# Optimization experiments

Hardware: AMD Instinct MI355X
Metric: run time of the kernel (lower is better)

Reference implementation:

```python
import jax, jax.numpy as jnp
import numpy as np

N_NODES = 100000
N_EDGES = 3200000
IN_C, HID_C, OUT_C = 128, 64, 64


def setup_inputs() -> dict:
    key = jax.random.key(0)
    k = jax.random.split(key, 6)
    x = jax.random.normal(k[0], (N_NODES, IN_C), dtype=jnp.float32)
    edge_index = jax.random.randint(k[1], (2, N_EDGES), 0, N_NODES, dtype=jnp.int64)
    edge_weight = jax.random.uniform(k[2], (N_EDGES,), dtype=jnp.float32)
    W1 = jax.random.normal(k[3], (IN_C, HID_C), dtype=jnp.float32) * (1.0 / np.sqrt(IN_C))
    b1 = jnp.zeros((HID_C,), dtype=jnp.float32)
    W2 = jax.random.normal(k[4], (HID_C, OUT_C), dtype=jnp.float32) * (1.0 / np.sqrt(HID_C))
    b2 = jnp.zeros((OUT_C,), dtype=jnp.float32)
    return {"x": x, "edge_index": edge_index, "edge_weight": edge_weight,
            "W1": W1, "b1": b1, "W2": W2, "b2": b2}


def _gcn_norm(edge_index, edge_weight, num_nodes, dtype):
    # PyG GCNConv default: add self-loops (weight 1), symmetric normalization
    loop = jnp.arange(num_nodes, dtype=edge_index.dtype)
    row = jnp.concatenate([edge_index[0], loop])  # sources
    col = jnp.concatenate([edge_index[1], loop])  # targets (aggregation dim)
    w = jnp.concatenate([edge_weight.astype(dtype), jnp.ones((num_nodes,), dtype)])
    deg = jax.ops.segment_sum(w, col, num_segments=num_nodes)
    deg_inv_sqrt = jnp.where(deg > 0, jax.lax.rsqrt(deg), jnp.zeros((), dtype))
    norm = deg_inv_sqrt[row] * w * deg_inv_sqrt[col]
    return row, col, norm


def _gcn_conv(h, row, col, norm, W, b, num_nodes):
    h = h @ W                      # [N, C_out]
    msg = h[row] * norm[:, None]   # gather over sources, scale by edge norm
    out = jax.ops.segment_sum(msg, col, num_segments=num_nodes)  # scatter-add to targets
    return out + b


def reference(x, edge_index, edge_weight, W1, b1, W2, b2):
    num_nodes = x.shape[0]
    row, col, norm = _gcn_norm(edge_index, edge_weight, num_nodes, x.dtype)
    h = _gcn_conv(x, row, col, norm, W1, b1, num_nodes)
    h = jax.nn.relu(h)
    return _gcn_conv(h, row, col, norm, W2, b2, num_nodes)
```

## Files before the change

kernel.cpp:

```cpp
#include <hip/hip_runtime.h>
#include <hip/hip_bf16.h>

#define N_NODES 100000
#define N_EDGES 3200000
#define IN_C 128
#define HID_C 64
#define OUT_C 64

#define NBUCKET 196
#define SC_EDGES 4096
#define SC_GRID 782
#define CAP 18432

struct EdgeRec { int s; float v; };

typedef float f32x2 __attribute__((ext_vector_type(2)));
typedef float f32x4 __attribute__((ext_vector_type(4)));
typedef short bf16x8 __attribute__((ext_vector_type(8)));
union F8 { uint4 u; bf16x8 f; };

__device__ __forceinline__ unsigned pack_bf16(float lo, float hi) {
    unsigned short l = __hip_bfloat16_raw(__float2bfloat16(lo)).x;
    unsigned short h = __hip_bfloat16_raw(__float2bfloat16(hi)).x;
    return ((unsigned)h << 16) | l;
}
__device__ __forceinline__ float bf_lo(unsigned u) {
    union { unsigned u; float f; } c; c.u = u << 16; return c.f;
}
__device__ __forceinline__ float bf_hi(unsigned u) {
    union { unsigned u; float f; } c; c.u = u & 0xffff0000u; return c.f;
}
__device__ __forceinline__ f32x2 bfp(unsigned u) {
    union { unsigned u; float f; } lo, hi;
    lo.u = u << 16; hi.u = u & 0xffff0000u;
    f32x2 r; r.x = lo.f; r.y = hi.f; return r;
}
__device__ __forceinline__ void pk_fma(f32x2& acc, f32x2 a, f32x2 w) {
    asm("v_pk_fma_f32 %0, %1, %2, %0" : "+v"(acc) : "v"(a), "v"(w));
}
__device__ __forceinline__ void edge_acc(f32x2* acc2, uint4 u, float w) {
    f32x2 wv; wv.x = w; wv.y = w;
    pk_fma(acc2[0], bfp(u.x), wv);
    pk_fma(acc2[1], bfp(u.y), wv);
    pk_fma(acc2[2], bfp(u.z), wv);
    pk_fma(acc2[3], bfp(u.w), wv);
}
__device__ __forceinline__ unsigned cvt_pk_bf16(float lo, float hi) {
    unsigned r;
    asm("v_cvt_pk_bf16_f32 %0, %1, %2" : "=v"(r) : "v"(lo), "v"(hi));
    return r;
}
__device__ __forceinline__ void split_frag(const float* f, uint4& hi4, uint4& lo4) {
    unsigned hi[4], lo[4];
    #pragma unroll
    for (int p = 0; p < 4; ++p) {
        hi[p] = cvt_pk_bf16(f[2 * p], f[2 * p + 1]);
        float r0 = f[2 * p]     - bf_lo(hi[p]);
        float r1 = f[2 * p + 1] - bf_hi(hi[p]);
        lo[p] = cvt_pk_bf16(r0, r1);
    }
    hi4 = make_uint4(hi[0], hi[1], hi[2], hi[3]);
    lo4 = make_uint4(lo[0], lo[1], lo[2], lo[3]);
}

__global__ __launch_bounds__(256) void scatter_coarse(const int* __restrict__ ei,
                                                      const float* __restrict__ ew,
                                                      int* __restrict__ gcursor,
                                                      uint2* __restrict__ tmp) {
    __shared__ int hist[256];
    __shared__ int scan[256];
    __shared__ int lcur[256];
    __shared__ int adj[256];
    __shared__ uint2 rec[SC_EDGES];
    __shared__ unsigned char bk[SC_EDGES];
    int tid = threadIdx.x;
    hist[tid] = 0;
    __syncthreads();
    int base = blockIdx.x * SC_EDGES;
    unsigned ys[16];
    float    ws[16];
    int      bs[16];
    for (int i = 0; i < 16; ++i) {
        int e = base + i * 256 + tid;
        if (e < N_EDGES) {
            int t = ei[N_EDGES + e];
            bs[i] = t >> 9;
            ys[i] = (unsigned)ei[e] | ((unsigned)(t & 511) << 17);
            ws[i] = ew[e];
            atomicAdd(&hist[bs[i]], 1);
        } else bs[i] = -1;
    }
    __syncthreads();
    int v = hist[tid];
    scan[tid] = v;
    __syncthreads();
    for (int off = 1; off < 256; off <<= 1) {
        int t = scan[tid];
        int add = (tid >= off) ? scan[tid - off] : 0;
        __syncthreads();
        scan[tid] = t + add;
        __syncthreads();
    }
    int excl = scan[tid] - v;
    int gb = (v > 0) ? atomicAdd(&gcursor[tid], v) : 0;
    lcur[tid] = excl;
    adj[tid] = tid * CAP + gb - excl;
    __syncthreads();
    for (int i = 0; i < 16; ++i) {
        if (bs[i] >= 0) {
            int j = atomicAdd(&lcur[bs[i]], 1);
            rec[j] = make_uint2(__float_as_uint(ws[i]), ys[i]);
            bk[j] = (unsigned char)bs[i];
        }
    }
    __syncthreads();
    int count = N_EDGES - base;
    if (count > SC_EDGES) count = SC_EDGES;
    for (int j = tid; j < count; j += 256) {
        int b = bk[j];
        tmp[adj[b] + j] = rec[j];
    }
}

__global__ __launch_bounds__(256) void bucket_scan(const int* __restrict__ gcnt,
                                                   int* __restrict__ start) {
    __shared__ int s[256];
    int tid = threadIdx.x;
    int v = gcnt[tid];
    s[tid] = v;
    __syncthreads();
    for (int off = 1; off < 256; off <<= 1) {
        int t = s[tid];
        int add = (tid >= off) ? s[tid - off] : 0;
        __syncthreads();
        s[tid] = t + add;
        __syncthreads();
    }
    start[tid] = s[tid] - v;
    if (tid == 255) start[256] = s[255];
}

__global__ __launch_bounds__(512) void fine_sort(const int* __restrict__ start,
                                                 const uint2* __restrict__ tmpPad,
                                                 int* __restrict__ rowptr,
                                                 float* __restrict__ dis,
                                                 EdgeRec* __restrict__ ed) {
    __shared__ int   cnt[512];
    __shared__ float wdeg[512];
    __shared__ int   s[512];
    int tid = threadIdx.x;
    int nodeBase = blockIdx.x << 9;
    int bb = start[blockIdx.x];
    int nEdge = start[blockIdx.x + 1] - bb;
    const uint2* tb = tmpPad + (size_t)blockIdx.x * CAP;
    cnt[tid] = 0;
    wdeg[tid] = 0.f;
    __syncthreads();
    for (int e = tid; e < nEdge; e += 512) {
        uint2 r = tb[e];
        int l = (r.y >> 17) & 511;
        atomicAdd(&cnt[l], 1);
        atomicAdd(&wdeg[l], __uint_as_float(r.x));
    }
    __syncthreads();
    int v = cnt[tid];
    s[tid] = v;
    __syncthreads();
    for (int off = 1; off < 512; off <<= 1) {
        int t = s[tid];
        int add = (tid >= off) ? s[tid - off] : 0;
        __syncthreads();
        s[tid] = t + add;
        __syncthreads();
    }
    int excl = s[tid] - v;
    int node = nodeBase + tid;
    if (node < N_NODES) {
        rowptr[node] = bb + excl;
        dis[node] = rsqrtf(wdeg[tid] + 1.0f);
    }
    if (node == N_NODES) rowptr[N_NODES] = N_EDGES;
    cnt[tid] = excl;
    __syncthreads();
    for (int e = tid; e < nEdge; e += 512) {
        uint2 r = tb[e];
        int l = (r.y >> 17) & 511;
        int p = atomicAdd(&cnt[l], 1);
        EdgeRec o;
        o.s = (int)(r.y & 0x1FFFFu);
        o.v = __uint_as_float(r.x);
        ed[bb + p] = o;
    }
}

template<int K>
__global__ __launch_bounds__(256) void mm_mfma(const float* __restrict__ X,
                                               const float* __restrict__ W,
                                               const float* __restrict__ dis,
                                               unsigned* __restrict__ h) {
    constexpr int NKS = K / 32;
    int wv = threadIdx.x >> 6;
    int l  = threadIdx.x & 63;
    int lr = l & 15;
    int kr = l >> 4;
    int col = wv * 16 + lr;
    int row0 = blockIdx.x * 16;
    const float* xbase = X + (size_t)(row0 + lr) * K + kr * 8;
    float4 xa[NKS], xb[NKS];
    #pragma unroll
    for (int ks = 0; ks < NKS; ++ks) {
        const float4* xp = (const float4*)(xbase + ks * 32);
        xa[ks] = xp[0];
        xb[ks] = xp[1];
    }
    F8 bhi[NKS], blo[NKS];
    #pragma unroll
    for (int ks = 0; ks < NKS; ++ks) {
        const float* wp = W + (ks * 32 + kr * 8) * 64 + col;
        float f[8];
        #pragma unroll
        for (int j = 0; j < 8; ++j) f[j] = wp[j * 64];
        split_frag(f, bhi[ks].u, blo[ks].u);
    }
    f32x4 acc = {0.f, 0.f, 0.f, 0.f};
    #pragma unroll
    for (int ks = 0; ks < NKS; ++ks) {
        float f[8] = {xa[ks].x, xa[ks].y, xa[ks].z, xa[ks].w,
                      xb[ks].x, xb[ks].y, xb[ks].z, xb[ks].w};
        F8 ahi, alo;
        split_frag(f, ahi.u, alo.u);
        acc = __builtin_amdgcn_mfma_f32_16x16x32_bf16(ahi.f, bhi[ks].f, acc, 0, 0, 0);
        acc = __builtin_amdgcn_mfma_f32_16x16x32_bf16(ahi.f, blo[ks].f, acc, 0, 0, 0);
        acc = __builtin_amdgcn_mfma_f32_16x16x32_bf16(alo.f, bhi[ks].f, acc, 0, 0, 0);
    }
    int rbase = row0 + kr * 4;
    float v0 = acc[0] * dis[rbase + 0];
    float v1 = acc[1] * dis[rbase + 1];
    float v2 = acc[2] * dis[rbase + 2];
    float v3 = acc[3] * dis[rbase + 3];
    float o0 = __shfl_xor(v0, 1, 64);
    float o1 = __shfl_xor(v1, 1, 64);
    float o2 = __shfl_xor(v2, 1, 64);
    float o3 = __shfl_xor(v3, 1, 64);
    if ((lr & 1) == 0) {
        int ci = col >> 1;
        h[(rbase + 0) * 32 + ci] = pack_bf16(v0, o0);
        h[(rbase + 1) * 32 + ci] = pack_bf16(v1, o1);
        h[(rbase + 2) * 32 + ci] = pack_bf16(v2, o2);
        h[(rbase + 3) * 32 + ci] = pack_bf16(v3, o3);
    }
}

__global__ __launch_bounds__(256, 8) void agg_kernel(const int* __restrict__ rowptr,
                                                     const EdgeRec* __restrict__ ed,
                                                     const unsigned* __restrict__ h,
                                                     const float* __restrict__ dis,
                                                     const float* __restrict__ b,
                                                     float* __restrict__ out,
                                                     int relu) {
    int node = blockIdx.x * 4 + (threadIdx.x >> 6);
    int lane = threadIdx.x & 63;
    int g = lane >> 3;
    int cl = lane & 7;
    int beg = rowptr[node];
    int end = rowptr[node + 1];
    const uint4* h16 = (const uint4*)h;
    const char*  hb  = (const char*)h + (size_t)cl * 16;
    float d  = dis[node];
    uint4 us = h16[(size_t)node * 8 + cl];
    f32x2 acc2[4];
    acc2[0] = 0.f; acc2[1] = 0.f; acc2[2] = 0.f; acc2[3] = 0.f;
    int n = end - beg;
    int nb = (n + 31) >> 5;
    int nm1 = n - 1;
    uint2 q0, q1, q2, q3;
    if (nb > 0) {
        q0 = *(const uint2*)(ed + beg + min(g,      nm1));
        q1 = *(const uint2*)(ed + beg + min(g + 8,  nm1));
        q2 = *(const uint2*)(ed + beg + min(g + 16, nm1));
        q3 = *(const uint2*)(ed + beg + min(g + 24, nm1));
        for (int bt = 0; bt < nb; ++bt) {
            int ob = (bt << 5) + g;
            float w0 = (ob      < n) ? __uint_as_float(q0.y) : 0.f;
            float w1 = (ob + 8  < n) ? __uint_as_float(q1.y) : 0.f;
            float w2 = (ob + 16 < n) ? __uint_as_float(q2.y) : 0.f;
            float w3 = (ob + 24 < n) ? __uint_as_float(q3.y) : 0.f;
            uint4 u0 = *(const uint4*)(hb + ((size_t)(unsigned)q0.x << 7));
            uint4 u1 = *(const uint4*)(hb + ((size_t)(unsigned)q1.x << 7));
            uint4 u2 = *(const uint4*)(hb + ((size_t)(unsigned)q2.x << 7));
            uint4 u3 = *(const uint4*)(hb + ((size_t)(unsigned)q3.x << 7));
            if (bt + 1 < nb) {
                int on = ob + 32;
                q0 = *(const uint2*)(ed + beg + min(on,      nm1));
                q1 = *(const uint2*)(ed + beg + min(on + 8,  nm1));
                q2 = *(const uint2*)(ed + beg + min(on + 16, nm1));
                q3 = *(const uint2*)(ed + beg + min(on + 24, nm1));
            }
            edge_acc(acc2, u0, w0);
            edge_acc(acc2, u1, w1);
            edge_acc(acc2, u2, w2);
            edge_acc(acc2, u3, w3);
        }
    }
    float acc[8] = { acc2[0].x, acc2[0].y, acc2[1].x, acc2[1].y,
                     acc2[2].x, acc2[2].y, acc2[3].x, acc2[3].y };
    #pragma unroll
    for (int kk = 0; kk < 8; ++kk) {
        acc[kk] += __shfl_xor(acc[kk], 8, 64);
        acc[kk] += __shfl_xor(acc[kk], 16, 64);
        acc[kk] += __shfl_xor(acc[kk], 32, 64);
    }
    if (g == 0) {
        float hs[8] = { bf_lo(us.x), bf_hi(us.x), bf_lo(us.y), bf_hi(us.y),
                        bf_lo(us.z), bf_hi(us.z), bf_lo(us.w), bf_hi(us.w) };
        const float4* b4 = (const float4*)b;
        float4 bv0 = b4[cl * 2], bv1 = b4[cl * 2 + 1];
        float4 v0, v1;
        v0.x = d * (acc[0] + hs[0]) + bv0.x;
        v0.y = d * (acc[1] + hs[1]) + bv0.y;
        v0.z = d * (acc[2] + hs[2]) + bv0.z;
        v0.w = d * (acc[3] + hs[3]) + bv0.w;
        v1.x = d * (acc[4] + hs[4]) + bv1.x;
        v1.y = d * (acc[5] + hs[5]) + bv1.y;
        v1.z = d * (acc[6] + hs[6]) + bv1.z;
        v1.w = d * (acc[7] + hs[7]) + bv1.w;
        if (relu) {
            v0.x = fmaxf(v0.x, 0.f); v0.y = fmaxf(v0.y, 0.f);
            v0.z = fmaxf(v0.z, 0.f); v0.w = fmaxf(v0.w, 0.f);
            v1.x = fmaxf(v1.x, 0.f); v1.y = fmaxf(v1.y, 0.f);
            v1.z = fmaxf(v1.z, 0.f); v1.w = fmaxf(v1.w, 0.f);
        }
        float4* o4 = (float4*)out;
        o4[node * 16 + cl * 2]     = v0;
        o4[node * 16 + cl * 2 + 1] = v1;
    }
}

extern "C" void kernel_launch(void* const* d_in, const int* in_sizes, int n_in,
                              void* d_out, int out_size, void* d_ws, size_t ws_size,
                              hipStream_t stream) {
    const float* x  = (const float*)d_in[0];
    const int*   ei = (const int*)d_in[1];
    const float* ew = (const float*)d_in[2];
    const float* W1 = (const float*)d_in[3];
    const float* b1 = (const float*)d_in[4];
    const float* W2 = (const float*)d_in[5];
    const float* b2 = (const float*)d_in[6];
    float* out = (float*)d_out;

    char* p = (char*)d_ws;
    auto carve = [&](size_t bytes) { char* r = p; p += (bytes + 255) & ~(size_t)255; return r; };
    float*    dis     = (float*)carve(N_NODES * 4);
    int*      rowptr  = (int*)carve((N_NODES + 1) * 4);
    int*      start   = (int*)carve(257 * 4);
    int*      gcursor = (int*)carve(256 * 4);
    EdgeRec*  ed      = (EdgeRec*)carve((size_t)N_EDGES * 8);
    size_t    r2sz    = (size_t)NBUCKET * CAP * 8;
    size_t    hasz    = (size_t)N_NODES * 64 * 6;
    char*     r2      = carve(r2sz > hasz ? r2sz : hasz);
    uint2*    tmpPad  = (uint2*)r2;
    unsigned* h       = (unsigned*)r2;
    float*    a       = (float*)(r2 + (size_t)N_NODES * 64 * 2);

    hipMemsetAsync(gcursor, 0, 256 * sizeof(int), stream);
    scatter_coarse<<<SC_GRID, 256, 0, stream>>>(ei, ew, gcursor, tmpPad);
    bucket_scan<<<1, 256, 0, stream>>>(gcursor, start);
    fine_sort<<<NBUCKET, 512, 0, stream>>>(start, tmpPad, rowptr, dis, ed);

    mm_mfma<IN_C><<<N_NODES / 16, 256, 0, stream>>>(x, W1, dis, h);
    agg_kernel<<<N_NODES / 4, 256, 0, stream>>>(rowptr, ed, h, dis, b1, a, 1);

    mm_mfma<HID_C><<<N_NODES / 16, 256, 0, stream>>>(a, W2, dis, h);
    agg_kernel<<<N_NODES / 4, 256, 0, stream>>>(rowptr, ed, h, dis, b2, out, 0);
}
```

Baseline: 359.3 us.

## Compute degrees with global atomics and fuse first GEMM into coarse scatter

Adds a pass that computes per-node edge counts and weighted degrees with global atomics up front. The first matmul no longer waits on the sort, so its tiles run as extra blocks in the same launch as the coarse bucket scatter, overlapping compute with the scatter's memory traffic. The fine sort drops its counting pass and reads the precomputed counts, and later kernels recompute rsqrt from the weighted degree instead of reading a stored dis array. The trade is millions of contended global atomics and an extra read of the edge arrays, plus a larger workspace so h no longer aliases the scatter buffer.

Result: slower. 609.9 us (+69.8%).

```diff
diff --git a/kernel.cpp b/kernel.cpp
--- a/kernel.cpp
+++ b/kernel.cpp
@@ -11,6 +11,7 @@
 #define SC_EDGES 4096
 #define SC_GRID 782
 #define CAP 18432
+#define MM1_GRID (N_NODES / 16)
 
 struct EdgeRec { int s; float v; };
 
@@ -63,16 +64,96 @@
     lo4 = make_uint4(lo[0], lo[1], lo[2], lo[3]);
 }
 
-__global__ __launch_bounds__(256) void scatter_coarse(const int* __restrict__ ei,
-                                                      const float* __restrict__ ew,
-                                                      int* __restrict__ gcursor,
-                                                      uint2* __restrict__ tmp) {
+__global__ __launch_bounds__(256) void deg_kernel(const int* __restrict__ ei,
+                                                  const float* __restrict__ ew,
+                                                  int* __restrict__ deg,
+                                                  float* __restrict__ wdeg) {
+    int gid = blockIdx.x * 256 + threadIdx.x;
+    int4   t = ((const int4*)(ei + N_EDGES))[gid];
+    float4 w = ((const float4*)ew)[gid];
+    atomicAdd(&deg[t.x], 1); atomicAdd(&wdeg[t.x], w.x);
+    atomicAdd(&deg[t.y], 1); atomicAdd(&wdeg[t.y], w.y);
+    atomicAdd(&deg[t.z], 1); atomicAdd(&wdeg[t.z], w.z);
+    atomicAdd(&deg[t.w], 1); atomicAdd(&wdeg[t.w], w.w);
+}
+
+template<int K>
+__device__ __forceinline__ void mm_tile(int tile,
+                                        const float* __restrict__ X,
+                                        const float* __restrict__ W,
+                                        const float* __restrict__ wdeg,
+                                        unsigned* __restrict__ h) {
+    constexpr int NKS = K / 32;
+    int wv = threadIdx.x >> 6;
+    int l  = threadIdx.x & 63;
+    int lr = l & 15;
+    int kr = l >> 4;
+    int col = wv * 16 + lr;
+    int row0 = tile * 16;
+    const float* xbase = X + (size_t)(row0 + lr) * K + kr * 8;
+    float4 xa[NKS], xb[NKS];
+    #pragma unroll
+    for (int ks = 0; ks < NKS; ++ks) {
+        const float4* xp = (const float4*)(xbase + ks * 32);
+        xa[ks] = xp[0];
+        xb[ks] = xp[1];
+    }
+    F8 bhi[NKS], blo[NKS];
+    #pragma unroll
+    for (int ks = 0; ks < NKS; ++ks) {
+        const float* wp = W + (ks * 32 + kr * 8) * 64 + col;
+        float f[8];
+        #pragma unroll
+        for (int j = 0; j < 8; ++j) f[j] = wp[j * 64];
+        split_frag(f, bhi[ks].u, blo[ks].u);
+    }
+    f32x4 acc = {0.f, 0.f, 0.f, 0.f};
+    #pragma unroll
+    for (int ks = 0; ks < NKS; ++ks) {
+        float f[8] = {xa[ks].x, xa[ks].y, xa[ks].z, xa[ks].w,
+                      xb[ks].x, xb[ks].y, xb[ks].z, xb[ks].w};
+        F8 ahi, alo;
+        split_frag(f, ahi.u, alo.u);
+        acc = __builtin_amdgcn_mfma_f32_16x16x32_bf16(ahi.f, bhi[ks].f, acc, 0, 0, 0);
+        acc = __builtin_amdgcn_mfma_f32_16x16x32_bf16(ahi.f, blo[ks].f, acc, 0, 0, 0);
+        acc = __builtin_amdgcn_mfma_f32_16x16x32_bf16(alo.f, bhi[ks].f, acc, 0, 0, 0);
+    }
+    int rbase = row0 + kr * 4;
+    float v0 = acc[0] * rsqrtf(wdeg[rbase + 0] + 1.0f);
+    float v1 = acc[1] * rsqrtf(wdeg[rbase + 1] + 1.0f);
+    float v2 = acc[2] * rsqrtf(wdeg[rbase + 2] + 1.0f);
+    float v3 = acc[3] * rsqrtf(wdeg[rbase + 3] + 1.0f);
+    float o0 = __shfl_xor(v0, 1, 64);
+    float o1 = __shfl_xor(v1, 1, 64);
+    float o2 = __shfl_xor(v2, 1, 64);
+    float o3 = __shfl_xor(v3, 1, 64);
+    if ((lr & 1) == 0) {
+        int ci = col >> 1;
+        h[(rbase + 0) * 32 + ci] = pack_bf16(v0, o0);
+        h[(rbase + 1) * 32 + ci] = pack_bf16(v1, o1);
+        h[(rbase + 2) * 32 + ci] = pack_bf16(v2, o2);
+        h[(rbase + 3) * 32 + ci] = pack_bf16(v3, o3);
+    }
+}
+
+__global__ __launch_bounds__(256) void fused_scatter_mm1(const int* __restrict__ ei,
+                                                         const float* __restrict__ ew,
+                                                         int* __restrict__ gcursor,
+                                                         uint2* __restrict__ tmp,
+                                                         const float* __restrict__ x,
+                                                         const float* __restrict__ W1,
+                                                         const float* __restrict__ wdeg,
+                                                         unsigned* __restrict__ h) {
     __shared__ int hist[256];
     __shared__ int scan[256];
     __shared__ int lcur[256];
     __shared__ int adj[256];
     __shared__ uint2 rec[SC_EDGES];
     __shared__ unsigned char bk[SC_EDGES];
+    if (blockIdx.x >= SC_GRID) {
+        mm_tile<IN_C>(blockIdx.x - SC_GRID, x, W1, wdeg, h);
+        return;
+    }
     int tid = threadIdx.x;
     hist[tid] = 0;
     __syncthreads();
@@ -122,6 +203,14 @@
     }
 }
 
+template<int K>
+__global__ __launch_bounds__(256) void mm_mfma(const float* __restrict__ X,
+                                               const float* __restrict__ W,
+                                               const float* __restrict__ wdeg,
+                                               unsigned* __restrict__ h) {
+    mm_tile<K>(blockIdx.x, X, W, wdeg, h);
+}
+
 __global__ __launch_bounds__(256) void bucket_scan(const int* __restrict__ gcnt,
                                                    int* __restrict__ start) {
     __shared__ int s[256];
@@ -140,30 +229,20 @@
     if (tid == 255) start[256] = s[255];
 }
 
-__global__ __launch_bounds__(512) void fine_sort(const int* __restrict__ start,
-                                                 const uint2* __restrict__ tmpPad,
-                                                 int* __restrict__ rowptr,
-                                                 float* __restrict__ dis,
-                                                 EdgeRec* __restrict__ ed) {
-    __shared__ int   cnt[512];
-    __shared__ float wdeg[512];
-    __shared__ int   s[512];
+__global__ __launch_bounds__(512) void fine_place(const int* __restrict__ start,
+                                                  const int* __restrict__ deg,
+                                                  const uint2* __restrict__ tmpPad,
+                                                  int* __restrict__ rowptr,
+                                                  EdgeRec* __restrict__ ed) {
+    __shared__ int cnt[512];
+    __shared__ int s[512];
     int tid = threadIdx.x;
     int nodeBase = blockIdx.x << 9;
     int bb = start[blockIdx.x];
     int nEdge = start[blockIdx.x + 1] - bb;
     const uint2* tb = tmpPad + (size_t)blockIdx.x * CAP;
-    cnt[tid] = 0;
-    wdeg[tid] = 0.f;
-    __syncthreads();
-    for (int e = tid; e < nEdge; e += 512) {
-        uint2 r = tb[e];
-        int l = (r.y >> 17) & 511;
-        atomicAdd(&cnt[l], 1);
-        atomicAdd(&wdeg[l], __uint_as_float(r.x));
-    }
-    __syncthreads();
-    int v = cnt[tid];
+    int node = nodeBase + tid;
+    int v = (node < N_NODES) ? deg[node] : 0;
     s[tid] = v;
     __syncthreads();
     for (int off = 1; off < 512; off <<= 1) {
@@ -174,11 +253,7 @@
         __syncthreads();
     }
     int excl = s[tid] - v;
-    int node = nodeBase + tid;
-    if (node < N_NODES) {
-        rowptr[node] = bb + excl;
-        dis[node] = rsqrtf(wdeg[tid] + 1.0f);
-    }
+    if (node < N_NODES) rowptr[node] = bb + excl;
     if (node == N_NODES) rowptr[N_NODES] = N_EDGES;
     cnt[tid] = excl;
     __syncthreads();
@@ -193,68 +268,10 @@
     }
 }
 
-template<int K>
-__global__ __launch_bounds__(256) void mm_mfma(const float* __restrict__ X,
-                                               const float* __restrict__ W,
-                                               const float* __restrict__ dis,
-                                               unsigned* __restrict__ h) {
-    constexpr int NKS = K / 32;
-    int wv = threadIdx.x >> 6;
-    int l  = threadIdx.x & 63;
-    int lr = l & 15;
-    int kr = l >> 4;
-    int col = wv * 16 + lr;
-    int row0 = blockIdx.x * 16;
-    const float* xbase = X + (size_t)(row0 + lr) * K + kr * 8;
-    float4 xa[NKS], xb[NKS];
-    #pragma unroll
-    for (int ks = 0; ks < NKS; ++ks) {
-        const float4* xp = (const float4*)(xbase + ks * 32);
-        xa[ks] = xp[0];
-        xb[ks] = xp[1];
-    }
-    F8 bhi[NKS], blo[NKS];
-    #pragma unroll
-    for (int ks = 0; ks < NKS; ++ks) {
-        const float* wp = W + (ks * 32 + kr * 8) * 64 + col;
-        float f[8];
-        #pragma unroll
-        for (int j = 0; j < 8; ++j) f[j] = wp[j * 64];
-        split_frag(f, bhi[ks].u, blo[ks].u);
-    }
-    f32x4 acc = {0.f, 0.f, 0.f, 0.f};
-    #pragma unroll
-    for (int ks = 0; ks < NKS; ++ks) {
-        float f[8] = {xa[ks].x, xa[ks].y, xa[ks].z, xa[ks].w,
-                      xb[ks].x, xb[ks].y, xb[ks].z, xb[ks].w};
-        F8 ahi, alo;
-        split_frag(f, ahi.u, alo.u);
-        acc = __builtin_amdgcn_mfma_f32_16x16x32_bf16(ahi.f, bhi[ks].f, acc, 0, 0, 0);
-        acc = __builtin_amdgcn_mfma_f32_16x16x32_bf16(ahi.f, blo[ks].f, acc, 0, 0, 0);
-        acc = __builtin_amdgcn_mfma_f32_16x16x32_bf16(alo.f, bhi[ks].f, acc, 0, 0, 0);
-    }
-    int rbase = row0 + kr * 4;
-    float v0 = acc[0] * dis[rbase + 0];
-    float v1 = acc[1] * dis[rbase + 1];
-    float v2 = acc[2] * dis[rbase + 2];
-    float v3 = acc[3] * dis[rbase + 3];
-    float o0 = __shfl_xor(v0, 1, 64);
-    float o1 = __shfl_xor(v1, 1, 64);
-    float o2 = __shfl_xor(v2, 1, 64);
-    float o3 = __shfl_xor(v3, 1, 64);
-    if ((lr & 1) == 0) {
-        int ci = col >> 1;
-        h[(rbase + 0) * 32 + ci] = pack_bf16(v0, o0);
-        h[(rbase + 1) * 32 + ci] = pack_bf16(v1, o1);
-        h[(rbase + 2) * 32 + ci] = pack_bf16(v2, o2);
-        h[(rbase + 3) * 32 + ci] = pack_bf16(v3, o3);
-    }
-}
-
 __global__ __launch_bounds__(256, 8) void agg_kernel(const int* __restrict__ rowptr,
                                                      const EdgeRec* __restrict__ ed,
                                                      const unsigned* __restrict__ h,
-                                                     const float* __restrict__ dis,
+                                                     const float* __restrict__ wdeg,
                                                      const float* __restrict__ b,
                                                      float* __restrict__ out,
                                                      int relu) {
@@ -266,7 +283,7 @@
     int end = rowptr[node + 1];
     const uint4* h16 = (const uint4*)h;
     const char*  hb  = (const char*)h + (size_t)cl * 16;
-    float d  = dis[node];
+    float d  = rsqrtf(wdeg[node] + 1.0f);
     uint4 us = h16[(size_t)node * 8 + cl];
     f32x2 acc2[4];
     acc2[0] = 0.f; acc2[1] = 0.f; acc2[2] = 0.f; acc2[3] = 0.f;
@@ -350,26 +367,32 @@
 
     char* p = (char*)d_ws;
     auto carve = [&](size_t bytes) { char* r = p; p += (bytes + 255) & ~(size_t)255; return r; };
-    float*    dis     = (float*)carve(N_NODES * 4);
     int*      rowptr  = (int*)carve((N_NODES + 1) * 4);
     int*      start   = (int*)carve(257 * 4);
+    char*     z0      = p;
     int*      gcursor = (int*)carve(256 * 4);
+    int*      deg     = (int*)carve(N_NODES * 4);
+    float*    wdeg    = (float*)carve(N_NODES * 4);
+    size_t    zbytes  = (size_t)(p - z0);
     EdgeRec*  ed      = (EdgeRec*)carve((size_t)N_EDGES * 8);
+    unsigned* h       = (unsigned*)carve((size_t)N_NODES * 64 * 2);
     size_t    r2sz    = (size_t)NBUCKET * CAP * 8;
-    size_t    hasz    = (size_t)N_NODES * 64 * 6;
-    char*     r2      = carve(r2sz > hasz ? r2sz : hasz);
+    size_t    asz     = (size_t)N_NODES * 64 * 4;
+    char*     r2      = carve(r2sz > asz ? r2sz : asz);
     uint2*    tmpPad  = (uint2*)r2;
-    unsigned* h       = (unsigned*)r2;
-    float*    a       = (float*)(r2 + (size_t)N_NODES * 64 * 2);
-
-    hipMemsetAsync(gcursor, 0, 256 * sizeof(int), stream);
-    scatter_coarse<<<SC_GRID, 256, 0, stream>>>(ei, ew, gcursor, tmpPad);
+    float*    a       = (float*)r2;
+
+    hipMemsetAsync(z0, 0, zbytes, stream);
+
+    deg_kernel<<<N_EDGES / 1024, 256, 0, stream>>>(ei, ew, deg, wdeg);
+
+    fused_scatter_mm1<<<SC_GRID + MM1_GRID, 256, 0, stream>>>(ei, ew, gcursor,
+                                                              tmpPad, x, W1, wdeg, h);
     bucket_scan<<<1, 256, 0, stream>>>(gcursor, start);
-    fine_sort<<<NBUCKET, 512, 0, stream>>>(start, tmpPad, rowptr, dis, ed);
-
-    mm_mfma<IN_C><<<N_NODES / 16, 256, 0, stream>>>(x, W1, dis, h);
-    agg_kernel<<<N_NODES / 4, 256, 0, stream>>>(rowptr, ed, h, dis, b1, a, 1);
-
-    mm_mfma<HID_C><<<N_NODES / 16, 256, 0, stream>>>(a, W2, dis, h);
-    agg_kernel<<<N_NODES / 4, 256, 0, stream>>>(rowptr, ed, h, dis, b2, out, 0);
-}
+    fine_place<<<NBUCKET, 512, 0, stream>>>(start, deg, tmpPad, rowptr, ed);
+
+    agg_kernel<<<N_NODES / 4, 256, 0, stream>>>(rowptr, ed, h, wdeg, b1, a, 1);
+
+    mm_mfma<HID_C><<<N_NODES / 16, 256, 0, stream>>>(a, W2, wdeg, h);
+    agg_kernel<<<N_NODES / 4, 256, 0, stream>>>(rowptr, ed, h, wdeg, b2, out, 0);
+}
```

## Fuse first GEMM with edge scatter and fold source degree into edge weights

Applied to the files above, without the earlier changes.

The first projection X@W1 no longer depends on the degree normalization, so it runs as extra blocks inside the coarse edge-scatter launch, letting compute and the memory-bound scatter overlap. The source-side dis factor moves out of the GEMM epilogue into a new placement kernel that premultiplies each edge weight by dis[src]. The self-loop term is scaled by d in the aggregation instead. The fine sort splits into a count kernel and a place kernel, which adds a launch and re-reads tmpPad. The second GEMM uses a grid-stride loop with 1250 blocks and loads the weight fragments once per block.

After: 357.2 us. No clear change (-0.6%).

```diff
diff --git a/kernel.cpp b/kernel.cpp
--- a/kernel.cpp
+++ b/kernel.cpp
@@ -9,8 +9,10 @@
 
 #define NBUCKET 196
 #define SC_EDGES 4096
-#define SC_GRID 782
+#define SC_PER   (SC_EDGES / 256)
+#define SC_GRID  782
 #define CAP 18432
+#define MM1_GRID (N_NODES / 16)
 
 struct EdgeRec { int s; float v; };
 
@@ -63,24 +65,21 @@
     lo4 = make_uint4(lo[0], lo[1], lo[2], lo[3]);
 }
 
-__global__ __launch_bounds__(256) void scatter_coarse(const int* __restrict__ ei,
-                                                      const float* __restrict__ ew,
-                                                      int* __restrict__ gcursor,
-                                                      uint2* __restrict__ tmp) {
-    __shared__ int hist[256];
-    __shared__ int scan[256];
-    __shared__ int lcur[256];
-    __shared__ int adj[256];
-    __shared__ uint2 rec[SC_EDGES];
-    __shared__ unsigned char bk[SC_EDGES];
+__device__ __forceinline__ void scatter_body(const int* __restrict__ ei,
+                                             const float* __restrict__ ew,
+                                             int* __restrict__ gcursor,
+                                             uint2* __restrict__ tmp,
+                                             int* hist, int* scn, int* lcur,
+                                             int* adj, uint2* rec,
+                                             unsigned char* bk) {
     int tid = threadIdx.x;
     hist[tid] = 0;
     __syncthreads();
     int base = blockIdx.x * SC_EDGES;
-    unsigned ys[16];
-    float    ws[16];
-    int      bs[16];
-    for (int i = 0; i < 16; ++i) {
+    unsigned ys[SC_PER];
+    float    ws[SC_PER];
+    int      bs[SC_PER];
+    for (int i = 0; i < SC_PER; ++i) {
         int e = base + i * 256 + tid;
         if (e < N_EDGES) {
             int t = ei[N_EDGES + e];
@@ -92,21 +91,21 @@
     }
     __syncthreads();
     int v = hist[tid];
-    scan[tid] = v;
+    scn[tid] = v;
     __syncthreads();
     for (int off = 1; off < 256; off <<= 1) {
-        int t = scan[tid];
-        int add = (tid >= off) ? scan[tid - off] : 0;
-        __syncthreads();
-        scan[tid] = t + add;
-        __syncthreads();
-    }
-    int excl = scan[tid] - v;
+        int t = scn[tid];
+        int add = (tid >= off) ? scn[tid - off] : 0;
+        __syncthreads();
+        scn[tid] = t + add;
+        __syncthreads();
+    }
+    int excl = scn[tid] - v;
     int gb = (v > 0) ? atomicAdd(&gcursor[tid], v) : 0;
     lcur[tid] = excl;
     adj[tid] = tid * CAP + gb - excl;
     __syncthreads();
-    for (int i = 0; i < 16; ++i) {
+    for (int i = 0; i < SC_PER; ++i) {
         if (bs[i] >= 0) {
             int j = atomicAdd(&lcur[bs[i]], 1);
             rec[j] = make_uint2(__float_as_uint(ws[i]), ys[i]);
@@ -120,6 +119,101 @@
         int b = bk[j];
         tmp[adj[b] + j] = rec[j];
     }
+}
+
+template<int K>
+__device__ __forceinline__ void mm_tile_bf(int tile,
+                                           const float* __restrict__ X,
+                                           const F8* bhi, const F8* blo,
+                                           int lr, int kr, int col,
+                                           unsigned* __restrict__ h) {
+    constexpr int NKS = K / 32;
+    int row0 = tile * 16;
+    const float* xbase = X + (size_t)(row0 + lr) * K + kr * 8;
+    float4 xa[NKS], xb[NKS];
+    #pragma unroll
+    for (int ks = 0; ks < NKS; ++ks) {
+        const float4* xp = (const float4*)(xbase + ks * 32);
+        xa[ks] = xp[0];
+        xb[ks] = xp[1];
+    }
+    f32x4 acc = {0.f, 0.f, 0.f, 0.f};
+    #pragma unroll
+    for (int ks = 0; ks < NKS; ++ks) {
+        float f[8] = {xa[ks].x, xa[ks].y, xa[ks].z, xa[ks].w,
+                      xb[ks].x, xb[ks].y, xb[ks].z, xb[ks].w};
+        F8 ahi, alo;
+        split_frag(f, ahi.u, alo.u);
+        acc = __builtin_amdgcn_mfma_f32_16x16x32_bf16(ahi.f, bhi[ks].f, acc, 0, 0, 0);
+        acc = __builtin_amdgcn_mfma_f32_16x16x32_bf16(ahi.f, blo[ks].f, acc, 0, 0, 0);
+        acc = __builtin_amdgcn_mfma_f32_16x16x32_bf16(alo.f, bhi[ks].f, acc, 0, 0, 0);
+    }
+    int rbase = row0 + kr * 4;
+    float v0 = acc[0], v1 = acc[1], v2 = acc[2], v3 = acc[3];
+    float o0 = __shfl_xor(v0, 1, 64);
+    float o1 = __shfl_xor(v1, 1, 64);
+    float o2 = __shfl_xor(v2, 1, 64);
+    float o3 = __shfl_xor(v3, 1, 64);
+    if ((lr & 1) == 0) {
+        int ci = col >> 1;
+        h[(rbase + 0) * 32 + ci] = pack_bf16(v0, o0);
+        h[(rbase + 1) * 32 + ci] = pack_bf16(v1, o1);
+        h[(rbase + 2) * 32 + ci] = pack_bf16(v2, o2);
+        h[(rbase + 3) * 32 + ci] = pack_bf16(v3, o3);
+    }
+}
+
+template<int K>
+__device__ __forceinline__ void load_bfrags(const float* __restrict__ W,
+                                            int kr, int col, F8* bhi, F8* blo) {
+    #pragma unroll
+    for (int ks = 0; ks < K / 32; ++ks) {
+        const float* wp = W + (ks * 32 + kr * 8) * 64 + col;
+        float f[8];
+        #pragma unroll
+        for (int j = 0; j < 8; ++j) f[j] = wp[j * 64];
+        split_frag(f, bhi[ks].u, blo[ks].u);
+    }
+}
+
+__global__ __launch_bounds__(256) void fused_scatter_mm1(const int* __restrict__ ei,
+                                                         const float* __restrict__ ew,
+                                                         int* __restrict__ gcursor,
+                                                         uint2* __restrict__ tmp,
+                                                         const float* __restrict__ x,
+                                                         const float* __restrict__ W1,
+                                                         unsigned* __restrict__ h) {
+    __shared__ int hist[256];
+    __shared__ int scn[256];
+    __shared__ int lcur[256];
+    __shared__ int adj[256];
+    __shared__ uint2 rec[SC_EDGES];
+    __shared__ unsigned char bk[SC_EDGES];
+    if (blockIdx.x >= SC_GRID) {
+        int l  = threadIdx.x & 63;
+        int lr = l & 15;
+        int kr = l >> 4;
+        int col = (threadIdx.x >> 6) * 16 + lr;
+        F8 bhi[IN_C / 32], blo[IN_C / 32];
+        load_bfrags<IN_C>(W1, kr, col, bhi, blo);
+        mm_tile_bf<IN_C>(blockIdx.x - SC_GRID, x, bhi, blo, lr, kr, col, h);
+        return;
+    }
+    scatter_body(ei, ew, gcursor, tmp, hist, scn, lcur, adj, rec, bk);
+}
+
+template<int K>
+__global__ __launch_bounds__(256) void mm_mfma_raw(const float* __restrict__ X,
+                                                   const float* __restrict__ W,
+                                                   unsigned* __restrict__ h) {
+    int l  = threadIdx.x & 63;
+    int lr = l & 15;
+    int kr = l >> 4;
+    int col = (threadIdx.x >> 6) * 16 + lr;
+    F8 bhi[K / 32], blo[K / 32];
+    load_bfrags<K>(W, kr, col, bhi, blo);
+    for (int t = blockIdx.x; t < N_NODES / 16; t += gridDim.x)
+        mm_tile_bf<K>(t, X, bhi, blo, lr, kr, col, h);
 }
 
 __global__ __launch_bounds__(256) void bucket_scan(const int* __restrict__ gcnt,
@@ -140,11 +234,10 @@
     if (tid == 255) start[256] = s[255];
 }
 
-__global__ __launch_bounds__(512) void fine_sort(const int* __restrict__ start,
-                                                 const uint2* __restrict__ tmpPad,
-                                                 int* __restrict__ rowptr,
-                                                 float* __restrict__ dis,
-                                                 EdgeRec* __restrict__ ed) {
+__global__ __launch_bounds__(512) void fine_count(const int* __restrict__ start,
+                                                  const uint2* __restrict__ tmpPad,
+                                                  int* __restrict__ rowptr,
+                                                  float* __restrict__ dis) {
     __shared__ int   cnt[512];
     __shared__ float wdeg[512];
     __shared__ int   s[512];
@@ -180,74 +273,31 @@
         dis[node] = rsqrtf(wdeg[tid] + 1.0f);
     }
     if (node == N_NODES) rowptr[N_NODES] = N_EDGES;
-    cnt[tid] = excl;
+}
+
+__global__ __launch_bounds__(512) void fine_place(const int* __restrict__ start,
+                                                  const uint2* __restrict__ tmpPad,
+                                                  const int* __restrict__ rowptr,
+                                                  const float* __restrict__ dis,
+                                                  EdgeRec* __restrict__ ed) {
+    __shared__ int cnt[512];
+    int tid = threadIdx.x;
+    int nodeBase = blockIdx.x << 9;
+    int bb = start[blockIdx.x];
+    int nEdge = start[blockIdx.x + 1] - bb;
+    const uint2* tb = tmpPad + (size_t)blockIdx.x * CAP;
+    int node = nodeBase + tid;
+    cnt[tid] = ((node < N_NODES) ? rowptr[node] : N_EDGES) - bb;
     __syncthreads();
     for (int e = tid; e < nEdge; e += 512) {
         uint2 r = tb[e];
         int l = (r.y >> 17) & 511;
+        int src = (int)(r.y & 0x1FFFFu);
         int p = atomicAdd(&cnt[l], 1);
         EdgeRec o;
-        o.s = (int)(r.y & 0x1FFFFu);
-        o.v = __uint_as_float(r.x);
+        o.s = src;
+        o.v = __uint_as_float(r.x) * dis[src];
         ed[bb + p] = o;
-    }
-}
-
-template<int K>
-__global__ __launch_bounds__(256) void mm_mfma(const float* __restrict__ X,
-                                               const float* __restrict__ W,
-                                               const float* __restrict__ dis,
-                                               unsigned* __restrict__ h) {
-    constexpr int NKS = K / 32;
-    int wv = threadIdx.x >> 6;
-    int l  = threadIdx.x & 63;
-    int lr = l & 15;
-    int kr = l >> 4;
-    int col = wv * 16 + lr;
-    int row0 = blockIdx.x * 16;
-    const float* xbase = X + (size_t)(row0 + lr) * K + kr * 8;
-    float4 xa[NKS], xb[NKS];
-    #pragma unroll
-    for (int ks = 0; ks < NKS; ++ks) {
-        const float4* xp = (const float4*)(xbase + ks * 32);
-        xa[ks] = xp[0];
-        xb[ks] = xp[1];
-    }
-    F8 bhi[NKS], blo[NKS];
-    #pragma unroll
-    for (int ks = 0; ks < NKS; ++ks) {
-        const float* wp = W + (ks * 32 + kr * 8) * 64 + col;
-        float f[8];
-        #pragma unroll
-        for (int j = 0; j < 8; ++j) f[j] = wp[j * 64];
-        split_frag(f, bhi[ks].u, blo[ks].u);
-    }
-    f32x4 acc = {0.f, 0.f, 0.f, 0.f};
-    #pragma unroll
-    for (int ks = 0; ks < NKS; ++ks) {
-        float f[8] = {xa[ks].x, xa[ks].y, xa[ks].z, xa[ks].w,
-                      xb[ks].x, xb[ks].y, xb[ks].z, xb[ks].w};
-        F8 ahi, alo;
-        split_frag(f, ahi.u, alo.u);
-        acc = __builtin_amdgcn_mfma_f32_16x16x32_bf16(ahi.f, bhi[ks].f, acc, 0, 0, 0);
-        acc = __builtin_amdgcn_mfma_f32_16x16x32_bf16(ahi.f, blo[ks].f, acc, 0, 0, 0);
-        acc = __builtin_amdgcn_mfma_f32_16x16x32_bf16(alo.f, bhi[ks].f, acc, 0, 0, 0);
-    }
-    int rbase = row0 + kr * 4;
-    float v0 = acc[0] * dis[rbase + 0];
-    float v1 = acc[1] * dis[rbase + 1];
-    float v2 = acc[2] * dis[rbase + 2];
-    float v3 = acc[3] * dis[rbase + 3];
-    float o0 = __shfl_xor(v0, 1, 64);
-    float o1 = __shfl_xor(v1, 1, 64);
-    float o2 = __shfl_xor(v2, 1, 64);
-    float o3 = __shfl_xor(v3, 1, 64);
-    if ((lr & 1) == 0) {
-        int ci = col >> 1;
-        h[(rbase + 0) * 32 + ci] = pack_bf16(v0, o0);
-        h[(rbase + 1) * 32 + ci] = pack_bf16(v1, o1);
-        h[(rbase + 2) * 32 + ci] = pack_bf16(v2, o2);
-        h[(rbase + 3) * 32 + ci] = pack_bf16(v3, o3);
     }
 }
 
@@ -316,14 +366,14 @@
         const float4* b4 = (const float4*)b;
         float4 bv0 = b4[cl * 2], bv1 = b4[cl * 2 + 1];
         float4 v0, v1;
-        v0.x = d * (acc[0] + hs[0]) + bv0.x;
-        v0.y = d * (acc[1] + hs[1]) + bv0.y;
-        v0.z = d * (acc[2] + hs[2]) + bv0.z;
-        v0.w = d * (acc[3] + hs[3]) + bv0.w;
-        v1.x = d * (acc[4] + hs[4]) + bv1.x;
-        v1.y = d * (acc[5] + hs[5]) + bv1.y;
-        v1.z = d * (acc[6] + hs[6]) + bv1.z;
-        v1.w = d * (acc[7] + hs[7]) + bv1.w;
+        v0.x = d * (acc[0] + d * hs[0]) + bv0.x;
+        v0.y = d * (acc[1] + d * hs[1]) + bv0.y;
+        v0.z = d * (acc[2] + d * hs[2]) + bv0.z;
+        v0.w = d * (acc[3] + d * hs[3]) + bv0.w;
+        v1.x = d * (acc[4] + d * hs[4]) + bv1.x;
+        v1.y = d * (acc[5] + d * hs[5]) + bv1.y;
+        v1.z = d * (acc[6] + d * hs[6]) + bv1.z;
+        v1.w = d * (acc[7] + d * hs[7]) + bv1.w;
         if (relu) {
             v0.x = fmaxf(v0.x, 0.f); v0.y = fmaxf(v0.y, 0.f);
             v0.z = fmaxf(v0.z, 0.f); v0.w = fmaxf(v0.w, 0.f);
@@ -350,26 +400,28 @@
 
     char* p = (char*)d_ws;
     auto carve = [&](size_t bytes) { char* r = p; p += (bytes + 255) & ~(size_t)255; return r; };
-    float*    dis     = (float*)carve(N_NODES * 4);
     int*      rowptr  = (int*)carve((N_NODES + 1) * 4);
     int*      start   = (int*)carve(257 * 4);
     int*      gcursor = (int*)carve(256 * 4);
+    float*    dis     = (float*)carve(N_NODES * 4);
     EdgeRec*  ed      = (EdgeRec*)carve((size_t)N_EDGES * 8);
-    size_t    r2sz    = (size_t)NBUCKET * CAP * 8;
-    size_t    hasz    = (size_t)N_NODES * 64 * 6;
-    char*     r2      = carve(r2sz > hasz ? r2sz : hasz);
+    unsigned* h       = (unsigned*)carve((size_t)N_NODES * 64 * 2);
+    size_t    tmpsz   = (size_t)NBUCKET * CAP * 8;
+    size_t    asz     = (size_t)N_NODES * 64 * 4;
+    char*     r2      = carve(tmpsz > asz ? tmpsz : asz);
     uint2*    tmpPad  = (uint2*)r2;
-    unsigned* h       = (unsigned*)r2;
-    float*    a       = (float*)(r2 + (size_t)N_NODES * 64 * 2);
+    float*    a       = (float*)r2;
 
     hipMemsetAsync(gcursor, 0, 256 * sizeof(int), stream);
-    scatter_coarse<<<SC_GRID, 256, 0, stream>>>(ei, ew, gcursor, tmpPad);
+
+    fused_scatter_mm1<<<SC_GRID + MM1_GRID, 256, 0, stream>>>(ei, ew, gcursor,
+                                                              tmpPad, x, W1, h);
     bucket_scan<<<1, 256, 0, stream>>>(gcursor, start);
-    fine_sort<<<NBUCKET, 512, 0, stream>>>(start, tmpPad, rowptr, dis, ed);
-
-    mm_mfma<IN_C><<<N_NODES / 16, 256, 0, stream>>>(x, W1, dis, h);
+    fine_count<<<NBUCKET, 512, 0, stream>>>(start, tmpPad, rowptr, dis);
+    fine_place<<<NBUCKET, 512, 0, stream>>>(start, tmpPad, rowptr, dis, ed);
+
     agg_kernel<<<N_NODES / 4, 256, 0, stream>>>(rowptr, ed, h, dis, b1, a, 1);
 
-    mm_mfma<HID_C><<<N_NODES / 16, 256, 0, stream>>>(a, W2, dis, h);
+    mm_mfma_raw<HID_C><<<1250, 256, 0, stream>>>(a, W2, h);
     agg_kernel<<<N_NODES / 4, 256, 0, stream>>>(rowptr, ed, h, dis, b2, out, 0);
 }
```
